# Performance work log

Hardware: AMD Instinct MI355X
Metric: run time of the kernel (lower is better)

## Reference

```python
import jax, jax.numpy as jnp
import numpy as np

B, T, C, H = 8, 1024, 768, 12
D = C // H  # head_dim = 64


def setup_inputs() -> dict:
    key = jax.random.key(0)
    ks = jax.random.split(key, 6)
    s = 1.0 / np.sqrt(C)
    x = jax.random.normal(ks[0], (B, T, C), dtype=jnp.float32)
    Wq = jax.random.normal(ks[1], (C, C), dtype=jnp.float32) * s
    Wk = jax.random.normal(ks[2], (C, C), dtype=jnp.float32) * s
    Wv = jax.random.normal(ks[3], (C, C), dtype=jnp.float32) * s
    Wo = jax.random.normal(ks[4], (C, C), dtype=jnp.float32) * s
    bq = jnp.zeros((C,), jnp.float32)
    bk = jnp.zeros((C,), jnp.float32)
    bv = jnp.zeros((C,), jnp.float32)
    bo = jnp.zeros((C,), jnp.float32)
    # causal mask, broadcastable to [B, H, T, T]
    mask = jnp.tril(jnp.ones((T, T), dtype=bool))[None, None, :, :]
    return {"x": x, "mask": mask, "Wq": Wq, "bq": bq, "Wk": Wk, "bk": bk,
            "Wv": Wv, "bv": bv, "Wo": Wo, "bo": bo}


def reference(x, mask, Wq, bq, Wk, bk, Wv, bv, Wo, bo):
    # QKV projections: [B,T,C] @ [C,C] -> [B,T,C]
    q = x @ Wq + bq
    k = x @ Wk + bk
    v = x @ Wv + bv
    # split heads -> [B,H,T,D]
    q = q.reshape(B, T, H, D).transpose(0, 2, 1, 3)
    k = k.reshape(B, T, H, D).transpose(0, 2, 1, 3)
    v = v.reshape(B, T, H, D).transpose(0, 2, 1, 3)
    scale = 1.0 / jnp.sqrt(jnp.float32(D))
    scores = jnp.einsum('bhtd,bhsd->bhts', q, k) * scale  # [B,H,T,T]
    scores = jnp.where(mask, scores, jnp.float32(-1e9))
    attn = jax.nn.softmax(scores, axis=-1)
    out = jnp.einsum('bhts,bhsd->bhtd', attn, v)  # [B,H,T,D]
    out = out.transpose(0, 2, 1, 3).reshape(B, T, C)
    return out @ Wo + bo
```

## Files before the change

kernel.cpp:

```cpp
#include <hip/hip_runtime.h>
#include <hip/hip_bf16.h>

#define B 8
#define T 1024
#define C 768
#define H 12
#define D 64
#define M (B * T)

typedef unsigned short u16;
typedef unsigned int u32;
typedef __attribute__((ext_vector_type(8))) short bf16x8;
typedef __attribute__((ext_vector_type(4))) float f32x4;

__device__ __forceinline__ u16 f2bf(float f) {
  union { float f; u32 u; } c; c.f = f;
  u32 r = c.u + 0x7FFF + ((c.u >> 16) & 1);
  return (u16)(r >> 16);
}

__device__ __forceinline__ void gload16(const void* g, void* l) {
  __builtin_amdgcn_global_load_lds(
      (const __attribute__((address_space(1))) void*)g,
      (__attribute__((address_space(3))) void*)l, 16, 0, 0);
}

__device__ __forceinline__ int swzA(int row) {
  return (row & 3) ^ ((row >> 2) & 1);
}

__global__ __launch_bounds__(256) void xconv_kernel(const float* __restrict__ in,
                                                    u16* __restrict__ out, int n4) {
  int i = blockIdx.x * 256 + threadIdx.x;
  int stride = gridDim.x * 256;
  for (; i < n4; i += stride) {
    float4 v = ((const float4*)in)[i];
    ushort4 o;
    o.x = f2bf(v.x); o.y = f2bf(v.y); o.z = f2bf(v.z); o.w = f2bf(v.w);
    ((ushort4*)out)[i] = o;
  }
}

__global__ __launch_bounds__(256) void wtrans_kernel(const float* __restrict__ Wq,
                                                     const float* __restrict__ Wk,
                                                     const float* __restrict__ Wv,
                                                     const float* __restrict__ Wo,
                                                     u16* __restrict__ WtQKV,
                                                     u16* __restrict__ WoT) {
  __shared__ float t[32][33];
  const int z = blockIdx.z;
  const float* W = (z == 0) ? Wq : (z == 1) ? Wk : (z == 2) ? Wv : Wo;
  u16* dst = (z < 3) ? (WtQKV + (size_t)z * 768 * 768) : WoT;
  const int k0 = blockIdx.y * 32, n0 = blockIdx.x * 32;
  const int tx = threadIdx.x & 31, ty = threadIdx.x >> 5;
#pragma unroll
  for (int i = 0; i < 4; i++) {
    int r = ty * 4 + i;
    t[r][tx] = W[(size_t)(k0 + r) * 768 + n0 + tx];
  }
  __syncthreads();
#pragma unroll
  for (int i = 0; i < 4; i++) {
    int r = ty * 4 + i;
    dst[(size_t)(n0 + r) * 768 + k0 + tx] = f2bf(t[tx][r]);
  }
}

template <typename OutT, bool ROWBIAS>
__global__ __launch_bounds__(256) void gemm_mfma_kernel(
    const u16* __restrict__ A,
    const u16* __restrict__ Wt,
    const float* __restrict__ b0, const float* __restrict__ b1,
    OutT* __restrict__ o0, OutT* __restrict__ o1,
    int ldOut, float sc0, float sc1) {
  __shared__ u16 As[128 * 32];
  __shared__ u16 Bs[128 * 32];
  const int tid = threadIdx.x;
  const int w = tid >> 6, l = tid & 63;
  const int g = l >> 4, c = l & 15;
  const int m0 = blockIdx.y * 128;
  const int n0g = blockIdx.x * 128;
  const int seg = (!ROWBIAS && n0g >= 768) ? 1 : 0;
  const int n0 = n0g - seg * 768;
  const float* bias = (seg == 0) ? b0 : b1;
  OutT* out = (seg == 0) ? o0 : o1;
  const float sc = (seg == 0) ? sc0 : sc1;
  const int wr = (w >> 1) * 64, wc = (w & 1) * 64;

  f32x4 acc[4][4];
#pragma unroll
  for (int i = 0; i < 4; i++)
#pragma unroll
    for (int j = 0; j < 4; j++) acc[i][j] = f32x4{0.f, 0.f, 0.f, 0.f};

  for (int k0 = 0; k0 < 768; k0 += 32) {
    __syncthreads();
#pragma unroll
    for (int t = 0; t < 2; t++) {
      int ii = w * 2 + t;
      int e16 = ii * 64 + l;
      int row = e16 >> 2, slot = e16 & 3;
      int gs = slot ^ swzA(row);
      gload16(A + (size_t)(m0 + row) * 768 + k0 + gs * 8, (char*)As + ii * 1024);
    }
#pragma unroll
    for (int t = 0; t < 2; t++) {
      int ii = w * 2 + t;
      int e16 = ii * 64 + l;
      int row = e16 >> 2, slot = e16 & 3;
      int gs = slot ^ swzA(row);
      gload16(Wt + (size_t)(n0g + row) * 768 + k0 + gs * 8, (char*)Bs + ii * 1024);
    }
    __syncthreads();

    bf16x8 af[4], bfr[4];
#pragma unroll
    for (int i = 0; i < 4; i++) {
      int row = wr + i * 16 + c;
      int slot = g ^ swzA(row);
      af[i] = *(const bf16x8*)(As + row * 32 + slot * 8);
    }
#pragma unroll
    for (int j = 0; j < 4; j++) {
      int row = wc + j * 16 + c;
      int slot = g ^ swzA(row);
      bfr[j] = *(const bf16x8*)(Bs + row * 32 + slot * 8);
    }
#pragma unroll
    for (int i = 0; i < 4; i++)
#pragma unroll
      for (int j = 0; j < 4; j++)
        acc[i][j] = __builtin_amdgcn_mfma_f32_16x16x32_bf16(af[i], bfr[j], acc[i][j], 0, 0, 0);
  }

  float brow[4][4];
  if (ROWBIAS) {
#pragma unroll
    for (int i = 0; i < 4; i++)
#pragma unroll
      for (int r = 0; r < 4; r++)
        brow[i][r] = b0[m0 + wr + i * 16 + g * 4 + r];
  }
#pragma unroll
  for (int j = 0; j < 4; j++) {
    int col = n0 + wc + j * 16 + c;
    float bcol = ROWBIAS ? 0.f : bias[col];
#pragma unroll
    for (int i = 0; i < 4; i++) {
#pragma unroll
      for (int r = 0; r < 4; r++) {
        int row = m0 + wr + i * 16 + g * 4 + r;
        float v = (acc[i][j][r] + (ROWBIAS ? brow[i][r] : bcol)) * sc;
        if constexpr (sizeof(OutT) == 2) {
          ((u16*)out)[(size_t)row * ldOut + col] = f2bf(v);
        } else {
          ((float*)out)[(size_t)row * ldOut + col] = v;
        }
      }
    }
  }
}

__global__ __launch_bounds__(256) void attn_mfma_kernel(
    const u16* __restrict__ Qb, const u16* __restrict__ Kb,
    const u16* __restrict__ VT, u16* __restrict__ Ob) {
  __shared__ u16 Ks[128 * 64];
  __shared__ u16 Vs[64 * 128];
  __shared__ u16 Ps[4][16][132];

  const int tid = threadIdx.x;
  const int w = tid >> 6, l = tid & 63;
  const int g = l >> 4, c = l & 15;

  const int wg = blockIdx.x;
  const int logical = (wg & 7) * 192 + (wg >> 3);
  const int bh = logical >> 4;
  const int qi = 15 - (logical & 15);
  const int q0 = qi * 64;
  const int b = bh / H, h = bh % H;
  const int qw = q0 + w * 16;

  bf16x8 qf[2];
  {
    size_t base = (size_t)(b * T + qw + c) * C + h * D;
    qf[0] = *(const bf16x8*)(Qb + base + g * 8);
    qf[1] = *(const bf16x8*)(Qb + base + 32 + g * 8);
  }

  f32x4 acc[4];
#pragma unroll
  for (int j = 0; j < 4; j++) acc[j] = f32x4{0.f, 0.f, 0.f, 0.f};
  float m_i[4], l_p[4];
#pragma unroll
  for (int r = 0; r < 4; r++) { m_i[r] = -1e30f; l_p[r] = 0.f; }

  const int nt = q0 / 128 + 1;
  for (int it = 0; it < nt; it++) {
    const int s0 = it * 128;
    __syncthreads();
#pragma unroll
    for (int t = 0; t < 4; t++) {
      int ii = w * 4 + t;
      int e16 = ii * 64 + l;
      int row = e16 >> 3, slot = e16 & 7;
      int gs = slot ^ (row & 7);
      gload16(Kb + (size_t)(b * T + s0 + row) * C + h * D + gs * 8, (char*)Ks + ii * 1024);
    }
#pragma unroll
    for (int t = 0; t < 4; t++) {
      int ii = w * 4 + t;
      int e16 = ii * 64 + l;
      int row = e16 >> 4, slot = e16 & 15;
      int gs = slot ^ (row & 15);
      gload16(VT + (size_t)(h * D + row) * M + b * T + s0 + gs * 8, (char*)Vs + ii * 1024);
    }
    __syncthreads();

    const bool active = (s0 <= qw + 15);
    if (active) {
      f32x4 s[8];
#pragma unroll
      for (int f = 0; f < 8; f++) s[f] = f32x4{0.f, 0.f, 0.f, 0.f};
#pragma unroll
      for (int f = 0; f < 8; f++) {
        int kvrow = f * 16 + c;
#pragma unroll
        for (int kc = 0; kc < 2; kc++) {
          int slot = (kc * 4 + g) ^ (kvrow & 7);
          bf16x8 kf = *(const bf16x8*)(Ks + kvrow * 64 + slot * 8);
          s[f] = __builtin_amdgcn_mfma_f32_16x16x32_bf16(qf[kc], kf, s[f], 0, 0, 0);
        }
      }
      const bool partial = (s0 + 127 > qw);
      if (partial) {
#pragma unroll
        for (int r = 0; r < 4; r++) {
          int q = qw + g * 4 + r;
#pragma unroll
          for (int f = 0; f < 8; f++) {
            int kv = s0 + f * 16 + c;
            if (kv > q) s[f][r] = -1e30f;
          }
        }
      }
      float mx[4];
#pragma unroll
      for (int r = 0; r < 4; r++) {
        float mr = s[0][r];
#pragma unroll
        for (int f = 1; f < 8; f++) mr = fmaxf(mr, s[f][r]);
        mx[r] = mr;
      }
#pragma unroll
      for (int off = 1; off < 16; off <<= 1)
#pragma unroll
        for (int r = 0; r < 4; r++) mx[r] = fmaxf(mx[r], __shfl_xor(mx[r], off, 64));
      bool defer = true;
#pragma unroll
      for (int r = 0; r < 4; r++) defer = defer && (mx[r] <= m_i[r] + 8.0f);
      if (!__all(defer)) {
#pragma unroll
        for (int r = 0; r < 4; r++) {
          float mn = fmaxf(m_i[r], mx[r]);
          float rc = exp2f(m_i[r] - mn);
          m_i[r] = mn;
          l_p[r] *= rc;
#pragma unroll
          for (int j = 0; j < 4; j++) acc[j][r] *= rc;
        }
      }
#pragma unroll
      for (int r = 0; r < 4; r++) {
        float sum = 0.f;
#pragma unroll
        for (int f = 0; f < 8; f++) {
          float p = exp2f(s[f][r] - m_i[r]);
          s[f][r] = p;
          sum += p;
        }
        l_p[r] += sum;
#pragma unroll
        for (int f = 0; f < 8; f += 2) {
          __hip_bfloat162 h2 = __float22bfloat162_rn(make_float2(s[f][r], s[f + 1][r]));
          u32 pk = *(u32*)&h2;
          Ps[w][g * 4 + r][f * 16 + c] = (u16)pk;
          Ps[w][g * 4 + r][(f + 1) * 16 + c] = (u16)(pk >> 16);
        }
      }
#pragma unroll
      for (int kc = 0; kc < 4; kc++) {
        bf16x8 pf = *(const bf16x8*)(&Ps[w][c][kc * 32 + g * 8]);
#pragma unroll
        for (int j = 0; j < 4; j++) {
          bf16x8 vf = *(const bf16x8*)(Vs + (j * 16 + c) * 128 + (((kc * 4 + g) ^ c) * 8));
          acc[j] = __builtin_amdgcn_mfma_f32_16x16x32_bf16(pf, vf, acc[j], 0, 0, 0);
        }
      }
    }
  }

  float inv[4];
#pragma unroll
  for (int r = 0; r < 4; r++) {
    float v = l_p[r];
#pragma unroll
    for (int off = 1; off < 16; off <<= 1) v += __shfl_xor(v, off, 64);
    inv[r] = 1.f / v;
  }
#pragma unroll
  for (int j = 0; j < 4; j++) {
#pragma unroll
    for (int r = 0; r < 4; r++) {
      int row = qw + g * 4 + r;
      int col = j * 16 + c;
      Ob[(size_t)(b * T + row) * C + h * D + col] = f2bf(acc[j][r] * inv[r]);
    }
  }
}

extern "C" void kernel_launch(void* const* d_in, const int* in_sizes, int n_in,
                              void* d_out, int out_size, void* d_ws, size_t ws_size,
                              hipStream_t stream) {
  const float* x  = (const float*)d_in[0];
  const float* Wq = (const float*)d_in[2];
  const float* bq = (const float*)d_in[3];
  const float* Wk = (const float*)d_in[4];
  const float* bk = (const float*)d_in[5];
  const float* Wv = (const float*)d_in[6];
  const float* bv = (const float*)d_in[7];
  const float* Wo = (const float*)d_in[8];
  const float* bo = (const float*)d_in[9];
  float* out = (float*)d_out;

  const size_t MC2 = (size_t)M * C * 2;
  char* ws = (char*)d_ws;
  u16* xb    = (u16*)(ws);
  u16* WtQKV = (u16*)(ws + MC2);
  u16* WoT   = (u16*)(ws + MC2 + 3538944);
  u16* Qb    = (u16*)(ws + MC2 + 3538944 + 1179648);
  u16* Kb    = (u16*)((char*)Qb + MC2);
  u16* VT    = (u16*)((char*)Kb + MC2);
  u16* Ob    = (u16*)((char*)VT + MC2);
  u16* WvT   = WtQKV + 2 * 768 * 768;

  const float qscale = 0.125f * 1.4426950408889634f;

  xconv_kernel<<<2048, 256, 0, stream>>>(x, xb, M * C / 4);
  wtrans_kernel<<<dim3(24, 24, 4), 256, 0, stream>>>(Wq, Wk, Wv, Wo, WtQKV, WoT);
  gemm_mfma_kernel<u16, false><<<dim3(12, 64), 256, 0, stream>>>(
      xb, WtQKV, bq, bk, Qb, Kb, 768, qscale, 1.f);
  gemm_mfma_kernel<u16, true><<<dim3(64, 6), 256, 0, stream>>>(
      WvT, xb, bv, bv, VT, VT, M, 1.f, 1.f);
  attn_mfma_kernel<<<1536, 256, 0, stream>>>(Qb, Kb, VT, Ob);
  gemm_mfma_kernel<float, false><<<dim3(6, 64), 256, 0, stream>>>(
      Ob, WoT, bo, bo, out, out, 768, 1.f, 1.f);
}
```

Baseline: 139.3 us.

## Rewrite attention with 32x32x16 MFMA, transposed S, and register-resident P

Rewrites the attention kernel so each wave handles 32 query rows with 32x32x16 bf16 MFMAs. It computes S transposed (K as the A operand) so softmax row stats need only a single cross-half shuffle. P is passed to the PV MFMA through lane shuffles instead of an LDS round trip. The block now covers 128 queries with 64-key tiles, halving the grid. The goal is less LDS traffic, fewer reduction shuffles and more MFMA work per instruction, at the cost of fewer blocks, heavier register use and per-element shuffles for rescaling and output.

```diff
diff --git a/kernel.cpp b/kernel.cpp
--- a/kernel.cpp
+++ b/kernel.cpp
@@ -12,6 +12,7 @@
 typedef unsigned int u32;
 typedef __attribute__((ext_vector_type(8))) short bf16x8;
 typedef __attribute__((ext_vector_type(4))) float f32x4;
+typedef __attribute__((ext_vector_type(16))) float f32x16;
 
 __device__ __forceinline__ u16 f2bf(float f) {
   union { float f; u32 u; } c; c.f = f;
@@ -164,157 +165,151 @@
 __global__ __launch_bounds__(256) void attn_mfma_kernel(
     const u16* __restrict__ Qb, const u16* __restrict__ Kb,
     const u16* __restrict__ VT, u16* __restrict__ Ob) {
-  __shared__ u16 Ks[128 * 64];
-  __shared__ u16 Vs[64 * 128];
-  __shared__ u16 Ps[4][16][132];
+  __shared__ u16 Ks2[512 * 8];
+  __shared__ u16 Vs2[512 * 8];
 
   const int tid = threadIdx.x;
   const int w = tid >> 6, l = tid & 63;
-  const int g = l >> 4, c = l & 15;
+  const int q31 = l & 31, hi = l >> 5;
 
   const int wg = blockIdx.x;
-  const int logical = (wg & 7) * 192 + (wg >> 3);
-  const int bh = logical >> 4;
-  const int qi = 15 - (logical & 15);
-  const int q0 = qi * 64;
+  const int logical = (wg & 7) * 96 + (wg >> 3);
+  const int bh = logical >> 3;
+  const int qi = 7 - (logical & 7);
+  const int q0 = qi * 128;
   const int b = bh / H, h = bh % H;
-  const int qw = q0 + w * 16;
-
-  bf16x8 qf[2];
+  const int qw = q0 + w * 32;
+
+  bf16x8 qf[4];
   {
-    size_t base = (size_t)(b * T + qw + c) * C + h * D;
-    qf[0] = *(const bf16x8*)(Qb + base + g * 8);
-    qf[1] = *(const bf16x8*)(Qb + base + 32 + g * 8);
-  }
-
-  f32x4 acc[4];
-#pragma unroll
-  for (int j = 0; j < 4; j++) acc[j] = f32x4{0.f, 0.f, 0.f, 0.f};
-  float m_i[4], l_p[4];
-#pragma unroll
-  for (int r = 0; r < 4; r++) { m_i[r] = -1e30f; l_p[r] = 0.f; }
-
-  const int nt = q0 / 128 + 1;
+    size_t base = (size_t)(b * T + qw + q31) * C + h * D + hi * 8;
+#pragma unroll
+    for (int ks = 0; ks < 4; ks++)
+      qf[ks] = *(const bf16x8*)(Qb + base + ks * 16);
+  }
+
+  f32x16 oacc[2];
+#pragma unroll
+  for (int d = 0; d < 2; d++)
+#pragma unroll
+    for (int r = 0; r < 16; r++) oacc[d][r] = 0.f;
+  float m_i = -1e30f, l_p = 0.f;
+
+  const size_t kb_lane = (size_t)q31 * C + hi * 8;
+  const size_t vt_row = (size_t)(h * D + l) * M + b * T;
+
+  const int nt = q0 / 64 + 2;
   for (int it = 0; it < nt; it++) {
-    const int s0 = it * 128;
+    const int s0 = it * 64;
     __syncthreads();
-#pragma unroll
-    for (int t = 0; t < 4; t++) {
-      int ii = w * 4 + t;
-      int e16 = ii * 64 + l;
-      int row = e16 >> 3, slot = e16 & 7;
-      int gs = slot ^ (row & 7);
-      gload16(Kb + (size_t)(b * T + s0 + row) * C + h * D + gs * 8, (char*)Ks + ii * 1024);
-    }
-#pragma unroll
-    for (int t = 0; t < 4; t++) {
-      int ii = w * 4 + t;
-      int e16 = ii * 64 + l;
-      int row = e16 >> 4, slot = e16 & 15;
-      int gs = slot ^ (row & 15);
-      gload16(VT + (size_t)(h * D + row) * M + b * T + s0 + gs * 8, (char*)Vs + ii * 1024);
-    }
+    {
+      const u16* kt = Kb + (size_t)(b * T + s0) * C + h * D;
+#pragma unroll
+      for (int j = 0; j < 8; j++)
+        gload16(kt + (size_t)((j >> 2) * 32) * C + kb_lane + (j & 3) * 16,
+                (char*)Ks2 + j * 1024);
+    }
+#pragma unroll
+    for (int j = 0; j < 8; j++)
+      gload16(VT + vt_row + s0 + (j >> 1) * 16 + (j & 1) * 8,
+              (char*)Vs2 + j * 1024);
     __syncthreads();
 
-    const bool active = (s0 <= qw + 15);
-    if (active) {
-      f32x4 s[8];
-#pragma unroll
-      for (int f = 0; f < 8; f++) s[f] = f32x4{0.f, 0.f, 0.f, 0.f};
-#pragma unroll
-      for (int f = 0; f < 8; f++) {
-        int kvrow = f * 16 + c;
-#pragma unroll
-        for (int kc = 0; kc < 2; kc++) {
-          int slot = (kc * 4 + g) ^ (kvrow & 7);
-          bf16x8 kf = *(const bf16x8*)(Ks + kvrow * 64 + slot * 8);
-          s[f] = __builtin_amdgcn_mfma_f32_16x16x32_bf16(qf[kc], kf, s[f], 0, 0, 0);
+    if (s0 > qw + 31) continue;
+
+    f32x16 sA[2];
+#pragma unroll
+    for (int blk = 0; blk < 2; blk++) {
+#pragma unroll
+      for (int r = 0; r < 16; r++) sA[blk][r] = 0.f;
+#pragma unroll
+      for (int ks = 0; ks < 4; ks++) {
+        bf16x8 kf = *(const bf16x8*)(Ks2 + ((blk * 4 + ks) * 64 + l) * 8);
+        sA[blk] = __builtin_amdgcn_mfma_f32_32x32x16_bf16(kf, qf[ks], sA[blk], 0, 0, 0);
+      }
+    }
+
+    const bool partial = (s0 + 63 > qw);
+    const int q = qw + q31;
+    float pmax = -1e30f;
+#pragma unroll
+    for (int blk = 0; blk < 2; blk++)
+#pragma unroll
+      for (int r = 0; r < 16; r++) {
+        float v = sA[blk][r];
+        if (partial) {
+          int kv = s0 + blk * 32 + (r & 3) + ((r >> 2) << 3) + (hi << 2);
+          v = (kv <= q) ? v : -1e30f;
+          sA[blk][r] = v;
         }
-      }
-      const bool partial = (s0 + 127 > qw);
-      if (partial) {
-#pragma unroll
-        for (int r = 0; r < 4; r++) {
-          int q = qw + g * 4 + r;
-#pragma unroll
-          for (int f = 0; f < 8; f++) {
-            int kv = s0 + f * 16 + c;
-            if (kv > q) s[f][r] = -1e30f;
-          }
+        pmax = fmaxf(pmax, v);
+      }
+    pmax = fmaxf(pmax, __shfl_xor(pmax, 32, 64));
+
+    if (!__all(pmax <= m_i + 8.0f)) {
+      float mn = fmaxf(m_i, pmax);
+      float rc = exp2f(m_i - mn);
+      m_i = mn;
+      l_p *= rc;
+#pragma unroll
+      for (int r = 0; r < 16; r++) {
+        int src = (r & 3) + ((r >> 2) << 3) + (hi << 2);
+        float rcq = __shfl(rc, src, 64);
+        oacc[0][r] *= rcq;
+        oacc[1][r] *= rcq;
+      }
+    }
+
+#pragma unroll
+    for (int blk = 0; blk < 2; blk++) {
+      float pv[16];
+      float sum = 0.f;
+#pragma unroll
+      for (int r = 0; r < 16; r++) {
+        float e = exp2f(sA[blk][r] - m_i);
+        pv[r] = e;
+        sum += e;
+      }
+      l_p += sum;
+      u32 pk[8];
+#pragma unroll
+      for (int i = 0; i < 8; i++) {
+        __hip_bfloat162 h2 = __float22bfloat162_rn(make_float2(pv[2 * i], pv[2 * i + 1]));
+        pk[i] = *(u32*)&h2;
+      }
+#pragma unroll
+      for (int sl = 0; sl < 2; sl++) {
+        u32 a = pk[sl * 4 + 0], bb = pk[sl * 4 + 1];
+        u32 cc = pk[sl * 4 + 2], dd = pk[sl * 4 + 3];
+        u32 xa = __shfl_xor(a, 32, 64);
+        u32 xb = __shfl_xor(bb, 32, 64);
+        u32 xc = __shfl_xor(cc, 32, 64);
+        u32 xd = __shfl_xor(dd, 32, 64);
+        union { u32 u[4]; bf16x8 v; } pf;
+        pf.u[0] = hi ? xc : a;
+        pf.u[1] = hi ? xd : bb;
+        pf.u[2] = hi ? cc : xa;
+        pf.u[3] = hi ? dd : xb;
+        int ks = blk * 2 + sl;
+#pragma unroll
+        for (int dblk = 0; dblk < 2; dblk++) {
+          bf16x8 vf = *(const bf16x8*)(
+              Vs2 + (ks * 128 + hi * 64 + dblk * 32 + q31) * 8);
+          oacc[dblk] = __builtin_amdgcn_mfma_f32_32x32x16_bf16(pf.v, vf, oacc[dblk], 0, 0, 0);
         }
       }
-      float mx[4];
-#pragma unroll
-      for (int r = 0; r < 4; r++) {
-        float mr = s[0][r];
-#pragma unroll
-        for (int f = 1; f < 8; f++) mr = fmaxf(mr, s[f][r]);
-        mx[r] = mr;
-      }
-#pragma unroll
-      for (int off = 1; off < 16; off <<= 1)
-#pragma unroll
-        for (int r = 0; r < 4; r++) mx[r] = fmaxf(mx[r], __shfl_xor(mx[r], off, 64));
-      bool defer = true;
-#pragma unroll
-      for (int r = 0; r < 4; r++) defer = defer && (mx[r] <= m_i[r] + 8.0f);
-      if (!__all(defer)) {
-#pragma unroll
-        for (int r = 0; r < 4; r++) {
-          float mn = fmaxf(m_i[r], mx[r]);
-          float rc = exp2f(m_i[r] - mn);
-          m_i[r] = mn;
-          l_p[r] *= rc;
-#pragma unroll
-          for (int j = 0; j < 4; j++) acc[j][r] *= rc;
-        }
-      }
-#pragma unroll
-      for (int r = 0; r < 4; r++) {
-        float sum = 0.f;
-#pragma unroll
-        for (int f = 0; f < 8; f++) {
-          float p = exp2f(s[f][r] - m_i[r]);
-          s[f][r] = p;
-          sum += p;
-        }
-        l_p[r] += sum;
-#pragma unroll
-        for (int f = 0; f < 8; f += 2) {
-          __hip_bfloat162 h2 = __float22bfloat162_rn(make_float2(s[f][r], s[f + 1][r]));
-          u32 pk = *(u32*)&h2;
-          Ps[w][g * 4 + r][f * 16 + c] = (u16)pk;
-          Ps[w][g * 4 + r][(f + 1) * 16 + c] = (u16)(pk >> 16);
-        }
-      }
-#pragma unroll
-      for (int kc = 0; kc < 4; kc++) {
-        bf16x8 pf = *(const bf16x8*)(&Ps[w][c][kc * 32 + g * 8]);
-#pragma unroll
-        for (int j = 0; j < 4; j++) {
-          bf16x8 vf = *(const bf16x8*)(Vs + (j * 16 + c) * 128 + (((kc * 4 + g) ^ c) * 8));
-          acc[j] = __builtin_amdgcn_mfma_f32_16x16x32_bf16(pf, vf, acc[j], 0, 0, 0);
-        }
-      }
-    }
-  }
-
-  float inv[4];
-#pragma unroll
-  for (int r = 0; r < 4; r++) {
-    float v = l_p[r];
-#pragma unroll
-    for (int off = 1; off < 16; off <<= 1) v += __shfl_xor(v, off, 64);
-    inv[r] = 1.f / v;
-  }
-#pragma unroll
-  for (int j = 0; j < 4; j++) {
-#pragma unroll
-    for (int r = 0; r < 4; r++) {
-      int row = qw + g * 4 + r;
-      int col = j * 16 + c;
-      Ob[(size_t)(b * T + row) * C + h * D + col] = f2bf(acc[j][r] * inv[r]);
-    }
+    }
+  }
+
+  float lt = l_p + __shfl_xor(l_p, 32, 64);
+  float inv = 1.0f / lt;
+#pragma unroll
+  for (int r = 0; r < 16; r++) {
+    int src = (r & 3) + ((r >> 2) << 3) + (hi << 2);
+    float invq = __shfl(inv, src, 64);
+    size_t base = (size_t)(b * T + qw + src) * C + h * D + q31;
+    Ob[base] = f2bf(oacc[0][r] * invq);
+    Ob[base + 32] = f2bf(oacc[1][r] * invq);
   }
 }
 
@@ -351,7 +346,7 @@
       xb, WtQKV, bq, bk, Qb, Kb, 768, qscale, 1.f);
   gemm_mfma_kernel<u16, true><<<dim3(64, 6), 256, 0, stream>>>(
       WvT, xb, bv, bv, VT, VT, M, 1.f, 1.f);
-  attn_mfma_kernel<<<1536, 256, 0, stream>>>(Qb, Kb, VT, Ob);
+  attn_mfma_kernel<<<768, 256, 0, stream>>>(Qb, Kb, VT, Ob);
   gemm_mfma_kernel<float, false><<<dim3(6, 64), 256, 0, stream>>>(
       Ob, WoT, bo, bo, out, out, 768, 1.f, 1.f);
 }
```

Measured after the change: 191.6 us. +37.6%, slower.
